# Performance work log

Measured on AMD Instinct MI355X. Metric: run time of the kernel, lower is better.

The kernel has to match this reference:

```python
import jax, jax.numpy as jnp
import numpy as np

HEAD_SIZE = 128


def setup_inputs() -> dict:
    key = jax.random.key(0)
    k0, k1, k2, k3 = jax.random.split(key, 4)
    B, S, E, H = 4, 4096, 1024, HEAD_SIZE
    x = jax.random.normal(k0, (B, S, E), dtype=jnp.float32)
    scale = 1.0 / np.sqrt(E).astype(np.float32)
    Wq = jax.random.normal(k1, (E, H), dtype=jnp.float32) * scale
    Wk = jax.random.normal(k2, (E, H), dtype=jnp.float32) * scale
    Wv = jax.random.normal(k3, (E, H), dtype=jnp.float32) * scale
    k_mask = jnp.ones((B, S), dtype=jnp.int32)
    return {"x": x, "Wq": Wq, "Wk": Wk, "Wv": Wv, "k_mask": k_mask}


def reference(x, Wq, Wk, Wv, k_mask):
    # Self-attention path (kv=None), causal=True
    Q = x @ Wq  # [B, S, H]
    K = x @ Wk  # [B, S, H]
    V = x @ Wv  # [B, S, H]
    inv_sqrt_h = np.float32(1.0 / np.sqrt(HEAD_SIZE))
    att = jnp.einsum('bqh,bkh->bqk', Q, K) * inv_sqrt_h  # [B, S, S]
    neg_inf = jnp.float32(-jnp.inf)
    # padding mask over keys: [B, 1, S_k]
    att = jnp.where(k_mask[:, None, :] == 0, neg_inf, att)
    # causal mask: tril over (q_len, k_len)
    S = Q.shape[1]
    c_mask = jnp.tril(jnp.ones((S, S), dtype=bool))  # [S, S]
    att = jnp.where(c_mask[None, :, :], att, neg_inf)
    att = jax.nn.softmax(att, axis=-1)
    return att @ V  # [B, S, H]
```

## Files before the change

kernel.cpp:

```cpp
#include <hip/hip_runtime.h>
#include <hip/hip_bf16.h>

typedef unsigned short u16;
typedef __attribute__((ext_vector_type(8))) short bf16x8;
typedef __attribute__((ext_vector_type(4))) float f32x4;
typedef __attribute__((ext_vector_type(4))) unsigned short u16x4;

#define SQ 4096
#define HQ 128
#define NCHUNK 144

__device__ __forceinline__ u16 f2b(float f) {
  unsigned int u = __float_as_uint(f);
  unsigned int r = (u + 0x7fffu + ((u >> 16) & 1u)) >> 16;
  return (u16)r;
}

__device__ __forceinline__ u16 f2b_fast(float f) {
  __hip_bfloat16 h = __float2bfloat16(f);
  return __builtin_bit_cast(u16, h);
}

__device__ __forceinline__ float b2f(u16 v) {
  unsigned int u = ((unsigned int)v) << 16;
  return __uint_as_float(u);
}

__device__ __forceinline__ void gload_lds16(const void* gsrc, void* ldst) {
  __builtin_amdgcn_global_load_lds((const __attribute__((address_space(1))) void*)gsrc,
                                   (__attribute__((address_space(3))) void*)ldst, 16, 0, 0);
}

__global__ __launch_bounds__(256) void k_wt(const float* __restrict__ Wq, const float* __restrict__ Wk,
                                            const float* __restrict__ Wv, u16* __restrict__ wt) {
  int idx = blockIdx.x * 256 + threadIdx.x;
  int z = idx >> 17, r = idx & 131071, n = r >> 10, k = r & 1023;
  const float* W = (z == 0) ? Wq : (z == 1) ? Wk : Wv;
  wt[idx] = f2b(W[k * 128 + n]);
}

__global__ __launch_bounds__(256) void k_proj(const float* __restrict__ x, const u16* __restrict__ wt,
                                              u16* __restrict__ qb, u16* __restrict__ kb,
                                              u16* __restrict__ vt) {
  int mt = blockIdx.x, nh = blockIdx.y;
  int t = threadIdx.x;
  int w = t >> 6, lane = t & 63;
  int wm = w >> 1, wn = w & 1;
  int lr = lane & 15, lg = lane >> 4;

  __shared__ __align__(16) float Al[2][128 * 32];
  __shared__ __align__(16) u16 Bl[2][96 * 32];

  f32x4 acc[4][3];
#pragma unroll
  for (int i = 0; i < 4; ++i)
#pragma unroll
    for (int j = 0; j < 3; ++j) acc[i][j] = (f32x4){0.f, 0.f, 0.f, 0.f};

  const float* xbase = x + (long)(mt * 128) * 1024;
  const u16* wbase = wt + (long)(nh * 96) * 1024;

  auto stage_a = [&](int bufi, int k0) {
#pragma unroll
    for (int i = 0; i < 4; ++i) {
      int ci = i * 256 + t;
      int row = ci >> 3, ch = ci & 7;
      gload_lds16(xbase + (long)row * 1024 + k0 + ((ch ^ (row & 7)) << 2),
                  &Al[bufi][0] + ci * 4);
    }
  };
  auto stage_b = [&](int bufi, int k0) {
    {
      int ci = t;
      int row = ci >> 2, ch = ci & 3;
      gload_lds16(wbase + (long)row * 1024 + k0 + ((ch ^ ((row >> 1) & 3)) << 3),
                  &Bl[bufi][0] + ci * 8);
    }
    if (t < 128) {
      int ci = 256 + t;
      int row = ci >> 2, ch = ci & 3;
      gload_lds16(wbase + (long)row * 1024 + k0 + ((ch ^ ((row >> 1) & 3)) << 3),
                  &Bl[bufi][0] + ci * 8);
    }
  };

  stage_a(0, 0);
  stage_b(0, 0);
  __syncthreads();

  for (int ks = 0; ks < 32; ++ks) {
    int cur = ks & 1;
    if (ks + 1 < 32) {
      stage_a(cur ^ 1, (ks + 1) * 32);
      stage_b(cur ^ 1, (ks + 1) * 32);
    }
    bf16x8 af[4], bfr[3];
#pragma unroll
    for (int i = 0; i < 4; ++i) {
      int row = wm * 64 + i * 16 + lr;
      const float* Ap = &Al[cur][row * 32];
      int sz = row & 7;
      float4 fa = *(const float4*)(Ap + (((2 * lg) ^ sz) << 2));
      float4 fb = *(const float4*)(Ap + (((2 * lg + 1) ^ sz) << 2));
      bf16x8 v;
      v[0] = (short)f2b_fast(fa.x); v[1] = (short)f2b_fast(fa.y);
      v[2] = (short)f2b_fast(fa.z); v[3] = (short)f2b_fast(fa.w);
      v[4] = (short)f2b_fast(fb.x); v[5] = (short)f2b_fast(fb.y);
      v[6] = (short)f2b_fast(fb.z); v[7] = (short)f2b_fast(fb.w);
      af[i] = v;
    }
#pragma unroll
    for (int j = 0; j < 3; ++j) {
      int row = wn * 48 + j * 16 + lr;
      bfr[j] = *(const bf16x8*)(&Bl[cur][0] + row * 32 + ((lg ^ ((row >> 1) & 3)) << 3));
    }
#pragma unroll
    for (int i = 0; i < 4; ++i)
#pragma unroll
      for (int j = 0; j < 3; ++j)
        acc[i][j] = __builtin_amdgcn_mfma_f32_16x16x32_bf16(af[i], bfr[j], acc[i][j], 0, 0, 0);
    __syncthreads();
  }

#pragma unroll
  for (int i = 0; i < 4; ++i)
#pragma unroll
    for (int j = 0; j < 3; ++j)
#pragma unroll
      for (int r = 0; r < 4; ++r) {
        int m = mt * 128 + wm * 64 + i * 16 + lg * 4 + r;
        int col = nh * 96 + wn * 48 + j * 16 + lr;
        int z = col >> 7, cz = col & 127;
        u16 v = f2b(acc[i][j][r]);
        if (z == 0) qb[(long)m * 128 + cz] = v;
        else if (z == 1) kb[(long)m * 128 + cz] = v;
        else { int bb = m >> 12, sR = m & 4095; vt[(long)bb * 524288 + (long)cz * 4096 + sR] = v; }
      }
}

__global__ __launch_bounds__(512, 4) void k_attn(const u16* __restrict__ qb, const u16* __restrict__ kb,
                                                 const u16* __restrict__ vt, const int* __restrict__ kmask,
                                                 u16* __restrict__ po, float* __restrict__ pl) {
  const float SCALE_LOG2 = 0.08838834764831845f * 1.4426950408889634f;
  const float MFIX = 24.0f;
  int f = (NCHUNK - 1) - (int)blockIdx.x;
  int b = blockIdx.y;
  int qt2 = 0, cum = 0;
  while (cum + ((qt2 + 4) >> 2) <= f) { cum += (qt2 + 4) >> 2; ++qt2; }
  int kc = f - cum;
  int ntile = 2 * qt2 + 2;
  int kt0 = kc * 8;
  int kt1 = min(kt0 + 8, ntile);

  int t = threadIdx.x, w = t >> 6, lane = t & 63;
  int lr = lane & 15, lg = lane >> 4, sw = lr & 7;
  int qrow0 = qt2 * 128 + w * 16;
  const u16* Q = qb + ((long)(b * SQ + qrow0)) * HQ;
  const u16* K = kb + (long)b * SQ * HQ;
  const u16* V = vt + (long)b * HQ * SQ;
  const int* msk = kmask + b * SQ;

  __shared__ __align__(16) u16 Kl[2][64 * 128];
  __shared__ __align__(16) u16 Vl[2][128 * 64];
  __shared__ __align__(16) u16 plds[8][16 * 64];

  bf16x8 aq[4];
#pragma unroll
  for (int c = 0; c < 4; ++c) aq[c] = *(const bf16x8*)(Q + lr * HQ + c * 32 + lg * 8);

  bf16x8 ones;
#pragma unroll
  for (int e = 0; e < 8; ++e) ones[e] = (short)0x3F80;

  f32x4 o[8];
#pragma unroll
  for (int n = 0; n < 8; ++n) o[n] = (f32x4){0.f, 0.f, 0.f, 0.f};
  f32x4 l_acc = (f32x4){0.f, 0.f, 0.f, 0.f};

  auto stage = [&](int bufi, int kb0) {
    const u16* Kg = K + (long)kb0 * HQ;
    const u16* Vg = V + kb0;
#pragma unroll
    for (int i = 0; i < 2; ++i) {
      int ci = w * 2 + i;
      int o16 = ci * 64 + lane;
      int row = o16 >> 4, ch = o16 & 15;
      gload_lds16(Kg + row * HQ + ((ch ^ (row & 7)) << 3), &Kl[bufi][ci * 512]);
    }
#pragma unroll
    for (int i = 0; i < 2; ++i) {
      int ci = w * 2 + i;
      int o16 = ci * 64 + lane;
      int row = o16 >> 3, ch = o16 & 7;
      gload_lds16(Vg + (long)row * SQ + ((ch ^ (row & 7)) << 3), &Vl[bufi][ci * 512]);
    }
  };

  stage(0, kt0 * 64);
  __syncthreads();

  u16* pw = &plds[w][0];
  for (int kt = kt0; kt < kt1; ++kt) {
    int cur = (kt - kt0) & 1;
    int kb0 = kt * 64;
    if (kt + 1 < kt1) stage(cur ^ 1, kb0 + 64);

    if (kb0 <= qrow0 + 15) {
      f32x4 s[4];
#pragma unroll
      for (int h = 0; h < 4; ++h) {
        f32x4 acc = (f32x4){0.f, 0.f, 0.f, 0.f};
        const u16* Kp = &Kl[cur][(h * 16 + lr) * 128];
#pragma unroll
        for (int c = 0; c < 4; ++c) {
          bf16x8 bk = *(const bf16x8*)(Kp + (((c * 4 + lg) ^ sw) << 3));
          acc = __builtin_amdgcn_mfma_f32_16x16x32_bf16(aq[c], bk, acc, 0, 0, 0);
        }
        s[h] = acc;
      }
      float mf[4];
#pragma unroll
      for (int h = 0; h < 4; ++h) mf[h] = (msk[kb0 + h * 16 + lr] != 0) ? 1.0f : 0.0f;
      bool needc = (kb0 + 63 > qrow0);
#pragma unroll
      for (int r = 0; r < 4; ++r) {
        int row = lg * 4 + r;
        int qr = qrow0 + row;
#pragma unroll
        for (int h = 0; h < 4; ++h) {
          float p = __builtin_exp2f(fmaf(s[h][r], SCALE_LOG2, -MFIX)) * mf[h];
          if (needc) p = ((kb0 + h * 16 + lr) <= qr) ? p : 0.0f;
          int poff = row * 64 + ((((h * 2 + (lr >> 3)) ^ (row & 7))) << 3) + (lr & 7);
          pw[poff] = f2b_fast(p);
        }
      }
      bf16x8 ap0 = *(const bf16x8*)(pw + lr * 64 + ((lg ^ sw) << 3));
      bf16x8 ap1 = *(const bf16x8*)(pw + lr * 64 + (((4 + lg) ^ sw) << 3));
      l_acc = __builtin_amdgcn_mfma_f32_16x16x32_bf16(ap0, ones, l_acc, 0, 0, 0);
      l_acc = __builtin_amdgcn_mfma_f32_16x16x32_bf16(ap1, ones, l_acc, 0, 0, 0);
#pragma unroll
      for (int n = 0; n < 8; ++n) {
        const u16* Vp = &Vl[cur][(n * 16 + lr) * 64];
        bf16x8 bv0 = *(const bf16x8*)(Vp + ((lg ^ sw) << 3));
        bf16x8 bv1 = *(const bf16x8*)(Vp + (((4 + lg) ^ sw) << 3));
        o[n] = __builtin_amdgcn_mfma_f32_16x16x32_bf16(ap0, bv0, o[n], 0, 0, 0);
        o[n] = __builtin_amdgcn_mfma_f32_16x16x32_bf16(ap1, bv1, o[n], 0, 0, 0);
      }
    }
    __syncthreads();
  }

  long p = (long)b * NCHUNK + f;
  u16* pob = po + p * 16384;
#pragma unroll
  for (int n = 0; n < 8; ++n)
#pragma unroll
    for (int r = 0; r < 4; ++r)
      pob[(w * 16 + lg * 4 + r) * 128 + n * 16 + lr] = f2b_fast(o[n][r]);
  if (lr == 0) {
#pragma unroll
    for (int r = 0; r < 4; ++r) pl[p * 128 + w * 16 + lg * 4 + r] = l_acc[r];
  }
}

__global__ __launch_bounds__(256) void k_merge(const u16* __restrict__ po, const float* __restrict__ pl,
                                               float* __restrict__ out) {
  int qt2 = blockIdx.x, b = blockIdx.y;
  int nch = (qt2 + 4) >> 2;
  int pre = 0;
  for (int q = 0; q < qt2; ++q) pre += (q + 4) >> 2;
  long pbase = (long)b * NCHUNK + pre;
  int t = threadIdx.x;
  int row = t >> 1, c0 = (t & 1) * 64;
  float l = 0.f;
  for (int i = 0; i < nch; ++i) l += pl[(pbase + i) * 128 + row];
  float inv = 1.0f / l;
  const u16* p0 = po + pbase * 16384 + row * 128 + c0;
  float* orow = out + ((long)(b * SQ + qt2 * 128 + row)) * HQ + c0;
#pragma unroll
  for (int j = 0; j < 64; j += 4) {
    float acc0 = 0.f, acc1 = 0.f, acc2 = 0.f, acc3 = 0.f;
    for (int i = 0; i < nch; ++i) {
      u16x4 v = *(const u16x4*)(p0 + (long)i * 16384 + j);
      acc0 += b2f(v[0]); acc1 += b2f(v[1]); acc2 += b2f(v[2]); acc3 += b2f(v[3]);
    }
    float4 r = {acc0 * inv, acc1 * inv, acc2 * inv, acc3 * inv};
    *(float4*)(orow + j) = r;
  }
}

extern "C" void kernel_launch(void* const* d_in, const int* in_sizes, int n_in,
                              void* d_out, int out_size, void* d_ws, size_t ws_size,
                              hipStream_t stream) {
  const float* x  = (const float*)d_in[0];
  const float* Wq = (const float*)d_in[1];
  const float* Wk = (const float*)d_in[2];
  const float* Wv = (const float*)d_in[3];
  const int* kmask = (const int*)d_in[4];
  char* ws = (char*)d_ws;
  u16* wt = (u16*)(ws + 33554432);
  u16* qb = (u16*)(ws + 34340864);
  u16* kb = (u16*)(ws + 38535168);
  u16* vt = (u16*)(ws + 42729472);
  u16* po = (u16*)ws;
  float* pl = (float*)(ws + 31195136);
  float* out = (float*)d_out;

  k_wt<<<1536, 256, 0, stream>>>(Wq, Wk, Wv, wt);
  k_proj<<<dim3(128, 4), 256, 0, stream>>>(x, wt, qb, kb, vt);
  k_attn<<<dim3(NCHUNK, 4), 512, 0, stream>>>(qb, kb, vt, kmask, po, pl);
  k_merge<<<dim3(32, 4), 256, 0, stream>>>(po, pl, out);
}
```

Before: 125.7 us.

## Pre-convert x to bf16 in prep kernel and use 128-wide projection tiles

Result: slower. 134.3 us (+6.8%).

```diff
diff --git a/kernel.cpp b/kernel.cpp
--- a/kernel.cpp
+++ b/kernel.cpp
@@ -5,6 +5,7 @@
 typedef __attribute__((ext_vector_type(8))) short bf16x8;
 typedef __attribute__((ext_vector_type(4))) float f32x4;
 typedef __attribute__((ext_vector_type(4))) unsigned short u16x4;
+typedef __attribute__((ext_vector_type(8))) unsigned short u16x8v;
 
 #define SQ 4096
 #define HQ 128
@@ -31,93 +32,86 @@
                                    (__attribute__((address_space(3))) void*)ldst, 16, 0, 0);
 }
 
-__global__ __launch_bounds__(256) void k_wt(const float* __restrict__ Wq, const float* __restrict__ Wk,
-                                            const float* __restrict__ Wv, u16* __restrict__ wt) {
-  int idx = blockIdx.x * 256 + threadIdx.x;
-  int z = idx >> 17, r = idx & 131071, n = r >> 10, k = r & 1023;
-  const float* W = (z == 0) ? Wq : (z == 1) ? Wk : Wv;
-  wt[idx] = f2b(W[k * 128 + n]);
-}
-
-__global__ __launch_bounds__(256) void k_proj(const float* __restrict__ x, const u16* __restrict__ wt,
-                                              u16* __restrict__ qb, u16* __restrict__ kb,
-                                              u16* __restrict__ vt) {
+__global__ __launch_bounds__(256) void k_prep(const float* __restrict__ x,
+                                              const float* __restrict__ Wq, const float* __restrict__ Wk,
+                                              const float* __restrict__ Wv,
+                                              u16* __restrict__ xb, u16* __restrict__ wt) {
+  int bid = blockIdx.x;
+  if (bid < 8192) {
+    long i = ((long)bid * 256 + threadIdx.x) * 8;
+    float4 a = *(const float4*)(x + i);
+    float4 c = *(const float4*)(x + i + 4);
+    u16x8v o;
+    o[0] = f2b(a.x); o[1] = f2b(a.y); o[2] = f2b(a.z); o[3] = f2b(a.w);
+    o[4] = f2b(c.x); o[5] = f2b(c.y); o[6] = f2b(c.z); o[7] = f2b(c.w);
+    *(u16x8v*)(xb + i) = o;
+  } else {
+    int idx = (bid - 8192) * 256 + threadIdx.x;
+    int z = idx >> 17, r = idx & 131071, n = r >> 10, k = r & 1023;
+    const float* W = (z == 0) ? Wq : (z == 1) ? Wk : Wv;
+    wt[idx] = f2b(W[k * 128 + n]);
+  }
+}
+
+__global__ __launch_bounds__(256, 4) void k_proj(const u16* __restrict__ xb, const u16* __restrict__ wt,
+                                                 u16* __restrict__ qb, u16* __restrict__ kb,
+                                                 u16* __restrict__ vt) {
   int mt = blockIdx.x, nh = blockIdx.y;
   int t = threadIdx.x;
   int w = t >> 6, lane = t & 63;
   int wm = w >> 1, wn = w & 1;
   int lr = lane & 15, lg = lane >> 4;
 
-  __shared__ __align__(16) float Al[2][128 * 32];
-  __shared__ __align__(16) u16 Bl[2][96 * 32];
-
-  f32x4 acc[4][3];
+  __shared__ __align__(16) u16 Al[2][128 * 32];
+  __shared__ __align__(16) u16 Bl[2][128 * 32];
+
+  f32x4 acc[4][4];
 #pragma unroll
   for (int i = 0; i < 4; ++i)
 #pragma unroll
-    for (int j = 0; j < 3; ++j) acc[i][j] = (f32x4){0.f, 0.f, 0.f, 0.f};
-
-  const float* xbase = x + (long)(mt * 128) * 1024;
-  const u16* wbase = wt + (long)(nh * 96) * 1024;
-
-  auto stage_a = [&](int bufi, int k0) {
-#pragma unroll
-    for (int i = 0; i < 4; ++i) {
+    for (int j = 0; j < 4; ++j) acc[i][j] = (f32x4){0.f, 0.f, 0.f, 0.f};
+
+  const u16* xbase = xb + (long)(mt * 128) * 1024;
+  const u16* wbase = wt + (long)(nh * 128) * 1024;
+
+  auto stage = [&](int bufi, int k0) {
+#pragma unroll
+    for (int i = 0; i < 2; ++i) {
       int ci = i * 256 + t;
-      int row = ci >> 3, ch = ci & 7;
-      gload_lds16(xbase + (long)row * 1024 + k0 + ((ch ^ (row & 7)) << 2),
-                  &Al[bufi][0] + ci * 4);
-    }
-  };
-  auto stage_b = [&](int bufi, int k0) {
-    {
-      int ci = t;
+      int row = ci >> 2, ch = ci & 3;
+      gload_lds16(xbase + (long)row * 1024 + k0 + ((ch ^ ((row >> 1) & 3)) << 3),
+                  &Al[bufi][0] + ci * 8);
+    }
+#pragma unroll
+    for (int i = 0; i < 2; ++i) {
+      int ci = i * 256 + t;
       int row = ci >> 2, ch = ci & 3;
       gload_lds16(wbase + (long)row * 1024 + k0 + ((ch ^ ((row >> 1) & 3)) << 3),
                   &Bl[bufi][0] + ci * 8);
     }
-    if (t < 128) {
-      int ci = 256 + t;
-      int row = ci >> 2, ch = ci & 3;
-      gload_lds16(wbase + (long)row * 1024 + k0 + ((ch ^ ((row >> 1) & 3)) << 3),
-                  &Bl[bufi][0] + ci * 8);
-    }
   };
 
-  stage_a(0, 0);
-  stage_b(0, 0);
+  stage(0, 0);
   __syncthreads();
 
   for (int ks = 0; ks < 32; ++ks) {
     int cur = ks & 1;
-    if (ks + 1 < 32) {
-      stage_a(cur ^ 1, (ks + 1) * 32);
-      stage_b(cur ^ 1, (ks + 1) * 32);
-    }
-    bf16x8 af[4], bfr[3];
+    if (ks + 1 < 32) stage(cur ^ 1, (ks + 1) * 32);
+    bf16x8 af[4], bfr[4];
 #pragma unroll
     for (int i = 0; i < 4; ++i) {
       int row = wm * 64 + i * 16 + lr;
-      const float* Ap = &Al[cur][row * 32];
-      int sz = row & 7;
-      float4 fa = *(const float4*)(Ap + (((2 * lg) ^ sz) << 2));
-      float4 fb = *(const float4*)(Ap + (((2 * lg + 1) ^ sz) << 2));
-      bf16x8 v;
-      v[0] = (short)f2b_fast(fa.x); v[1] = (short)f2b_fast(fa.y);
-      v[2] = (short)f2b_fast(fa.z); v[3] = (short)f2b_fast(fa.w);
-      v[4] = (short)f2b_fast(fb.x); v[5] = (short)f2b_fast(fb.y);
-      v[6] = (short)f2b_fast(fb.z); v[7] = (short)f2b_fast(fb.w);
-      af[i] = v;
-    }
-#pragma unroll
-    for (int j = 0; j < 3; ++j) {
-      int row = wn * 48 + j * 16 + lr;
+      af[i] = *(const bf16x8*)(&Al[cur][0] + row * 32 + ((lg ^ ((row >> 1) & 3)) << 3));
+    }
+#pragma unroll
+    for (int j = 0; j < 4; ++j) {
+      int row = wn * 64 + j * 16 + lr;
       bfr[j] = *(const bf16x8*)(&Bl[cur][0] + row * 32 + ((lg ^ ((row >> 1) & 3)) << 3));
     }
 #pragma unroll
     for (int i = 0; i < 4; ++i)
 #pragma unroll
-      for (int j = 0; j < 3; ++j)
+      for (int j = 0; j < 4; ++j)
         acc[i][j] = __builtin_amdgcn_mfma_f32_16x16x32_bf16(af[i], bfr[j], acc[i][j], 0, 0, 0);
     __syncthreads();
   }
@@ -125,15 +119,14 @@
 #pragma unroll
   for (int i = 0; i < 4; ++i)
 #pragma unroll
-    for (int j = 0; j < 3; ++j)
+    for (int j = 0; j < 4; ++j)
 #pragma unroll
       for (int r = 0; r < 4; ++r) {
         int m = mt * 128 + wm * 64 + i * 16 + lg * 4 + r;
-        int col = nh * 96 + wn * 48 + j * 16 + lr;
-        int z = col >> 7, cz = col & 127;
+        int cz = wn * 64 + j * 16 + lr;
         u16 v = f2b(acc[i][j][r]);
-        if (z == 0) qb[(long)m * 128 + cz] = v;
-        else if (z == 1) kb[(long)m * 128 + cz] = v;
+        if (nh == 0) qb[(long)m * 128 + cz] = v;
+        else if (nh == 1) kb[(long)m * 128 + cz] = v;
         else { int bb = m >> 12, sR = m & 4095; vt[(long)bb * 524288 + (long)cz * 4096 + sR] = v; }
       }
 }
@@ -298,6 +291,7 @@
   const float* Wv = (const float*)d_in[3];
   const int* kmask = (const int*)d_in[4];
   char* ws = (char*)d_ws;
+  u16* xb = (u16*)ws;
   u16* wt = (u16*)(ws + 33554432);
   u16* qb = (u16*)(ws + 34340864);
   u16* kb = (u16*)(ws + 38535168);
@@ -306,8 +300,8 @@
   float* pl = (float*)(ws + 31195136);
   float* out = (float*)d_out;
 
-  k_wt<<<1536, 256, 0, stream>>>(Wq, Wk, Wv, wt);
-  k_proj<<<dim3(128, 4), 256, 0, stream>>>(x, wt, qb, kb, vt);
+  k_prep<<<9728, 256, 0, stream>>>(x, Wq, Wk, Wv, xb, wt);
+  k_proj<<<dim3(128, 3), 256, 0, stream>>>(xb, wt, qb, kb, vt);
   k_attn<<<dim3(NCHUNK, 4), 512, 0, stream>>>(qb, kb, vt, kmask, po, pl);
   k_merge<<<dim3(32, 4), 256, 0, stream>>>(po, pl, out);
 }
```
